# Kernel tuning notes

Measured on AMD Instinct MI355X. Metric: run time of the kernel, lower is better.

Reference implementation:

```python
import jax, jax.numpy as jnp
import numpy as np

N_NODES = 10000
N_EDGES = 640000
HIDDEN = 128
OUT = 10

def setup_inputs() -> dict:
    key = jax.random.key(0)
    k1, k2, k3, k4 = jax.random.split(key, 4)
    x = jax.random.normal(k1, (N_NODES, HIDDEN), dtype=jnp.float32)
    edge_index = jax.random.randint(k2, (2, N_EDGES), 0, N_NODES, dtype=jnp.int64)
    # ClassifierMLP2 params: Linear(2*hidden -> hidden) -> ReLU -> Linear(hidden -> out)
    W1 = jax.random.normal(k3, (2 * HIDDEN, HIDDEN), dtype=jnp.float32) / np.sqrt(2 * HIDDEN)
    b1 = jnp.zeros((HIDDEN,), dtype=jnp.float32)
    W2 = jax.random.normal(k4, (HIDDEN, OUT), dtype=jnp.float32) / np.sqrt(HIDDEN)
    b2 = jnp.zeros((OUT,), dtype=jnp.float32)
    return {"x": x, "edge_index": edge_index, "W1": W1, "b1": b1, "W2": W2, "b2": b2}

def reference(x, edge_index, W1, b1, W2, b2):
    # mix_node_features(..., node_feat_mixing='cat'): gather src/dst node
    # embeddings per edge and concatenate along feature dim -> [E, 2*H]
    src, dst = edge_index[0], edge_index[1]
    edges_x = jnp.concatenate([x[src], x[dst]], axis=-1)  # [E, 2H]
    # ClassifierMLP2 (dropout inactive at inference)
    h = jax.nn.relu(edges_x @ W1 + b1)                    # [E, H]
    return h @ W2 + b2                                    # [E, OUT]
```

## Files before the change

### kernel.cpp

```cpp
#include <hip/hip_runtime.h>


typedef __fp16 h2 __attribute__((ext_vector_type(2)));
typedef __fp16 h8 __attribute__((ext_vector_type(8)));

#define HID  128
#define TWOH 256
#define OUTD 10
#define NPB  16
#define EPG  4

__global__ __launch_bounds__(256) void precompute_AB(
    const float* __restrict__ x,
    const float* __restrict__ W1,
    const float* __restrict__ b1,
    __fp16* __restrict__ AB,
    int n_nodes)
{
    __shared__ float xs[NPB][HID];
    const int t = threadIdx.x;
    const int node0 = blockIdx.x * NPB;

    const float4* xg = (const float4*)(x + (long)node0 * HID);
    float4* xs4 = (float4*)xs;
#pragma unroll
    for (int i = 0; i < (NPB * HID / 4) / 256; ++i)
        xs4[t + i * 256] = xg[t + i * 256];
    __syncthreads();

    const float* wcol = (t < HID) ? (W1 + t) : (W1 + HID * HID + (t - HID));

    float acc[NPB];
#pragma unroll
    for (int n = 0; n < NPB; ++n) acc[n] = 0.f;

    for (int k = 0; k < HID; ++k) {
        const float w = wcol[(long)k * HID];
#pragma unroll
        for (int n = 0; n < NPB; ++n)
            acc[n] = fmaf(xs[n][k], w, acc[n]);
    }

    const float bias = (t < HID) ? b1[t] : 0.f;
#pragma unroll
    for (int n = 0; n < NPB; ++n) {
        const int node = node0 + n;
        if (node < n_nodes) AB[(long)node * TWOH + t] = (__fp16)(acc[n] + bias);
    }
}

__global__ __launch_bounds__(256) void edge_mlp(
    const __fp16* __restrict__ AB,
    const int* __restrict__ ei,
    const float* __restrict__ W2,
    const float* __restrict__ b2,
    float* __restrict__ out,
    int n_edges)
{
    __shared__ h2 w2s[HID / 2][12];
    const int t = threadIdx.x;
    for (int i = t; i < (HID / 2) * OUTD; i += 256) {
        const int kp = i / OUTD, j = i % OUTD;
        h2 v;
        v.x = (__fp16)W2[(2 * kp) * OUTD + j];
        v.y = (__fp16)W2[(2 * kp + 1) * OUTD + j];
        w2s[kp][j] = v;
    }
    __syncthreads();

    const int l = t & 3;
    const int g = t >> 2;
    const long blockbase = (long)blockIdx.x * (64 * EPG);

    const float2 bl    = *(const float2*)(b2 + 2 * l);
    const float2 btail = *(const float2*)(b2 + 8);

    int sn[EPG], dn[EPG];
    bool valid[EPG];
#pragma unroll
    for (int i = 0; i < EPG; ++i) {
        const long e = blockbase + (long)i * 64 + g;
        valid[i] = (e < n_edges);
        const long ec = valid[i] ? e : 0;
        sn[i] = ei[ec];
        dn[i] = ei[(long)n_edges + ec];
    }

#pragma unroll
    for (int i = 0; i < EPG; ++i) {
        if (!valid[i]) continue;
        const long e = blockbase + (long)i * 64 + g;

        const h8* Arow = (const h8*)(AB + (long)sn[i] * TWOH);
        const h8* Brow = (const h8*)(AB + (long)dn[i] * TWOH + HID);

        const h8 a0 = Arow[l],      b0 = Brow[l];
        const h8 a1 = Arow[4 + l],  b1v = Brow[4 + l];
        const h8 a2 = Arow[8 + l],  b2v = Brow[8 + l];
        const h8 a3 = Arow[12 + l], b3v = Brow[12 + l];

        float acc[OUTD];
#pragma unroll
        for (int j = 0; j < OUTD; ++j) acc[j] = 0.f;

        const h8 z = {0, 0, 0, 0, 0, 0, 0, 0};
        h8 sچ[4];
        sچ[0] = __builtin_elementwise_max(a0 + b0, z);
        sچ[1] = __builtin_elementwise_max(a1 + b1v, z);
        sچ[2] = __builtin_elementwise_max(a2 + b2v, z);
        sچ[3] = __builtin_elementwise_max(a3 + b3v, z);

#pragma unroll
        for (int ii = 0; ii < 4; ++ii) {
            const h8 s = sچ[ii];
#pragma unroll
            for (int p = 0; p < 4; ++p) {
                const int kp = 16 * ii + 4 * l + p;
                const uint4 wa = *(const uint4*)&w2s[kp][0];
                const uint4 wb = *(const uint4*)&w2s[kp][4];
                const uint2 wc = *(const uint2*)&w2s[kp][8];
                const unsigned wv[10] = {wa.x, wa.y, wa.z, wa.w,
                                         wb.x, wb.y, wb.z, wb.w,
                                         wc.x, wc.y};
                h2 hp;
                hp.x = s[2 * p]; hp.y = s[2 * p + 1];
#pragma unroll
                for (int j = 0; j < OUTD; ++j) {
                    const h2 w = __builtin_bit_cast(h2, wv[j]);
                    acc[j] = __builtin_amdgcn_fdot2(hp, w, acc[j], false);
                }
            }
        }

#pragma unroll
        for (int j = 0; j < OUTD; ++j) {
            acc[j] += __shfl_xor(acc[j], 1);
            acc[j] += __shfl_xor(acc[j], 2);
        }

        float* o = out + e * OUTD;
        *(float2*)(o + 2 * l) = make_float2(acc[2 * l] + bl.x, acc[2 * l + 1] + bl.y);
        if (l == 0)
            *(float2*)(o + 8) = make_float2(acc[8] + btail.x, acc[9] + btail.y);
    }
}

extern "C" void kernel_launch(void* const* d_in, const int* in_sizes, int n_in,
                              void* d_out, int out_size, void* d_ws, size_t ws_size,
                              hipStream_t stream) {
    const float* x  = (const float*)d_in[0];
    const int*   ei = (const int*)d_in[1];
    const float* W1 = (const float*)d_in[2];
    const float* b1 = (const float*)d_in[3];
    const float* W2 = (const float*)d_in[4];
    const float* b2 = (const float*)d_in[5];
    float* out = (float*)d_out;

    const int n_nodes = in_sizes[0] / HID;
    const int n_edges = in_sizes[1] / 2;

    __fp16* AB = (__fp16*)d_ws;

    precompute_AB<<<(n_nodes + NPB - 1) / NPB, 256, 0, stream>>>(x, W1, b1, AB, n_nodes);

    const int edges_per_block = 64 * EPG;
    edge_mlp<<<(n_edges + edges_per_block - 1) / edges_per_block, 256, 0, stream>>>(
        AB, ei, W2, b2, out, n_edges);
}
```

Baseline: 61.88 us.

## Use 8 lanes per edge with register-resident W2 and vectorized node GEMM

The edge kernel now assigns 8 lanes per edge instead of 4, with 8 edges per wave per iteration and 256 edges per block. Each lane holds its slice of W2 in registers, which removes repeated LDS reads inside the per-edge loop. Edge indices are loaded inside the loop rather than prefetched, and a third shuffle stage is added to the reduction. The node precompute kernel reads x in float4 chunks with four W1 loads per step to cut LDS load instructions, at the cost of more registers and one fewer level of index prefetch.

```diff
diff --git a/kernel.cpp b/kernel.cpp
--- a/kernel.cpp
+++ b/kernel.cpp
@@ -8,9 +8,9 @@
 #define TWOH 256
 #define OUTD 10
 #define NPB  16
-#define EPG  4
+#define EPG  8
 
-__global__ __launch_bounds__(256) void precompute_AB(
+__global__ __launch_bounds__(256) void node_AB(
     const float* __restrict__ x,
     const float* __restrict__ W1,
     const float* __restrict__ b1,
@@ -34,11 +34,21 @@
 #pragma unroll
     for (int n = 0; n < NPB; ++n) acc[n] = 0.f;
 
-    for (int k = 0; k < HID; ++k) {
-        const float w = wcol[(long)k * HID];
+    for (int kb = 0; kb < HID / 4; ++kb) {
+        const float w0 = wcol[(long)(4 * kb + 0) * HID];
+        const float w1 = wcol[(long)(4 * kb + 1) * HID];
+        const float w2 = wcol[(long)(4 * kb + 2) * HID];
+        const float w3 = wcol[(long)(4 * kb + 3) * HID];
 #pragma unroll
-        for (int n = 0; n < NPB; ++n)
-            acc[n] = fmaf(xs[n][k], w, acc[n]);
+        for (int n = 0; n < NPB; ++n) {
+            const float4 xv = *(const float4*)&xs[n][kb * 4];
+            float a = acc[n];
+            a = fmaf(xv.x, w0, a);
+            a = fmaf(xv.y, w1, a);
+            a = fmaf(xv.z, w2, a);
+            a = fmaf(xv.w, w3, a);
+            acc[n] = a;
+        }
     }
 
     const float bias = (t < HID) ? b1[t] : 0.f;
@@ -57,10 +67,10 @@
     float* __restrict__ out,
     int n_edges)
 {
-    __shared__ h2 w2s[HID / 2][12];
+    __shared__ h2 w2s[HID / 2][OUTD];
     const int t = threadIdx.x;
-    for (int i = t; i < (HID / 2) * OUTD; i += 256) {
-        const int kp = i / OUTD, j = i % OUTD;
+    for (int m = t; m < (HID / 2) * OUTD; m += 256) {
+        const int kp = m / OUTD, j = m % OUTD;
         h2 v;
         v.x = (__fp16)W2[(2 * kp) * OUTD + j];
         v.y = (__fp16)W2[(2 * kp + 1) * OUTD + j];
@@ -68,80 +78,72 @@
     }
     __syncthreads();
 
-    const int l = t & 3;
-    const int g = t >> 2;
-    const long blockbase = (long)blockIdx.x * (64 * EPG);
+    const int lane = t & 63;
+    const int ll = lane & 7;
+    const int g  = lane >> 3;
+    const int wv = t >> 6;
 
-    const float2 bl    = *(const float2*)(b2 + 2 * l);
-    const float2 btail = *(const float2*)(b2 + 8);
+    h2 wreg[8][OUTD];
+#pragma unroll
+    for (int r = 0; r < 8; ++r) {
+        const int kp = (r >> 2) * 32 + 4 * ll + (r & 3);
+#pragma unroll
+        for (int j = 0; j < OUTD; ++j) wreg[r][j] = w2s[kp][j];
+    }
 
-    int sn[EPG], dn[EPG];
-    bool valid[EPG];
-#pragma unroll
-    for (int i = 0; i < EPG; ++i) {
-        const long e = blockbase + (long)i * 64 + g;
-        valid[i] = (e < n_edges);
-        const long ec = valid[i] ? e : 0;
-        sn[i] = ei[ec];
-        dn[i] = ei[(long)n_edges + ec];
-    }
+    float bj0 = 0.f, bj1 = 0.f;
+    if (ll < 5) { bj0 = b2[2 * ll]; bj1 = b2[2 * ll + 1]; }
+
+    const h8* __restrict__ ABv = (const h8*)AB;
+    const long ebase = (long)blockIdx.x * 256 + wv * 64 + g;
 
 #pragma unroll
     for (int i = 0; i < EPG; ++i) {
-        if (!valid[i]) continue;
-        const long e = blockbase + (long)i * 64 + g;
+        const long e = ebase + (long)i * 8;
+        if (e >= n_edges) continue;
+        const int sn = ei[e];
+        const int dn = ei[(long)n_edges + e];
 
-        const h8* Arow = (const h8*)(AB + (long)sn[i] * TWOH);
-        const h8* Brow = (const h8*)(AB + (long)dn[i] * TWOH + HID);
+        const long ab = (long)sn * 32, bb = (long)dn * 32;
+        const h8 a0 = ABv[ab + ll];
+        const h8 a1 = ABv[ab + 8 + ll];
+        const h8 c0 = ABv[bb + 16 + ll];
+        const h8 c1 = ABv[bb + 24 + ll];
 
-        const h8 a0 = Arow[l],      b0 = Brow[l];
-        const h8 a1 = Arow[4 + l],  b1v = Brow[4 + l];
-        const h8 a2 = Arow[8 + l],  b2v = Brow[8 + l];
-        const h8 a3 = Arow[12 + l], b3v = Brow[12 + l];
+        const h8 z = {0, 0, 0, 0, 0, 0, 0, 0};
+        const h8 s0 = __builtin_elementwise_max(a0 + c0, z);
+        const h8 s1 = __builtin_elementwise_max(a1 + c1, z);
 
         float acc[OUTD];
 #pragma unroll
         for (int j = 0; j < OUTD; ++j) acc[j] = 0.f;
 
-        const h8 z = {0, 0, 0, 0, 0, 0, 0, 0};
-        h8 sچ[4];
-        sچ[0] = __builtin_elementwise_max(a0 + b0, z);
-        sچ[1] = __builtin_elementwise_max(a1 + b1v, z);
-        sچ[2] = __builtin_elementwise_max(a2 + b2v, z);
-        sچ[3] = __builtin_elementwise_max(a3 + b3v, z);
-
 #pragma unroll
-        for (int ii = 0; ii < 4; ++ii) {
-            const h8 s = sچ[ii];
+        for (int p = 0; p < 4; ++p) {
+            h2 hp0; hp0.x = s0[2 * p]; hp0.y = s0[2 * p + 1];
+            h2 hp1; hp1.x = s1[2 * p]; hp1.y = s1[2 * p + 1];
 #pragma unroll
-            for (int p = 0; p < 4; ++p) {
-                const int kp = 16 * ii + 4 * l + p;
-                const uint4 wa = *(const uint4*)&w2s[kp][0];
-                const uint4 wb = *(const uint4*)&w2s[kp][4];
-                const uint2 wc = *(const uint2*)&w2s[kp][8];
-                const unsigned wv[10] = {wa.x, wa.y, wa.z, wa.w,
-                                         wb.x, wb.y, wb.z, wb.w,
-                                         wc.x, wc.y};
-                h2 hp;
-                hp.x = s[2 * p]; hp.y = s[2 * p + 1];
+            for (int j = 0; j < OUTD; ++j)
+                acc[j] = __builtin_amdgcn_fdot2(hp0, wreg[p][j], acc[j], false);
 #pragma unroll
-                for (int j = 0; j < OUTD; ++j) {
-                    const h2 w = __builtin_bit_cast(h2, wv[j]);
-                    acc[j] = __builtin_amdgcn_fdot2(hp, w, acc[j], false);
-                }
-            }
+            for (int j = 0; j < OUTD; ++j)
+                acc[j] = __builtin_amdgcn_fdot2(hp1, wreg[4 + p][j], acc[j], false);
         }
 
 #pragma unroll
         for (int j = 0; j < OUTD; ++j) {
             acc[j] += __shfl_xor(acc[j], 1);
             acc[j] += __shfl_xor(acc[j], 2);
+            acc[j] += __shfl_xor(acc[j], 4);
         }
 
-        float* o = out + e * OUTD;
-        *(float2*)(o + 2 * l) = make_float2(acc[2 * l] + bl.x, acc[2 * l + 1] + bl.y);
-        if (l == 0)
-            *(float2*)(o + 8) = make_float2(acc[8] + btail.x, acc[9] + btail.y);
+        if (ll < 5) {
+            const float v0 = (ll == 0) ? acc[0] : (ll == 1) ? acc[2]
+                           : (ll == 2) ? acc[4] : (ll == 3) ? acc[6] : acc[8];
+            const float v1 = (ll == 0) ? acc[1] : (ll == 1) ? acc[3]
+                           : (ll == 2) ? acc[5] : (ll == 3) ? acc[7] : acc[9];
+            *(float2*)(out + e * OUTD + 2 * ll) = make_float2(v0 + bj0, v1 + bj1);
+        }
     }
 }
 
@@ -161,9 +163,7 @@
 
     __fp16* AB = (__fp16*)d_ws;
 
-    precompute_AB<<<(n_nodes + NPB - 1) / NPB, 256, 0, stream>>>(x, W1, b1, AB, n_nodes);
+    node_AB<<<(n_nodes + NPB - 1) / NPB, 256, 0, stream>>>(x, W1, b1, AB, n_nodes);
 
-    const int edges_per_block = 64 * EPG;
-    edge_mlp<<<(n_edges + edges_per_block - 1) / edges_per_block, 256, 0, stream>>>(
-        AB, ei, W2, b2, out, n_edges);
+    edge_mlp<<<(n_edges + 255) / 256, 256, 0, stream>>>(AB, ei, W2, b2, out, n_edges);
 }
```

Result: slower. 70.99 us (+14.7%).
